# Kernel tuning notes

Measured on AMD Instinct MI355X. Metric: run time of the kernel, lower is better.

The kernel has to match this reference:

```python
import jax, jax.numpy as jnp
import numpy as np

B, J, D = 2048, 22, 128

def setup_inputs() -> dict:
    key = jax.random.key(0)
    k1, k2, k3 = jax.random.split(key, 3)
    src = jax.random.normal(k1, (B, J, D), dtype=jnp.float32)
    W = jax.random.normal(k2, (D, D), dtype=jnp.float32) * (1.0 / np.sqrt(D))
    b = jax.random.normal(k3, (D,), dtype=jnp.float32) * 0.01
    return {"src": src, "W": W, "b": b}

def reference(src, W, b):
    # Path-based accumulation sum_k (src[path[k+1]] - src[path[k]]) telescopes
    # to src[:, j, :] - src[:, i, :] for the shortest path i -> j.
    # pairwise[b, i, j, :] = src[b, j, :] - src[b, i, :]
    pairwise = src[:, None, :, :] - src[:, :, None, :]  # [B, J, J, D]
    # nn.Linear on last dim: x @ W^T + b
    return jnp.einsum('bijd,ed->bije', pairwise, W) + b
```

## Files before the change

kernel.cpp:

```cpp
#include <hip/hip_runtime.h>

#define NB 2048
#define NJ 22
#define ND 128
#define NBAT 8
#define NBLK (NB / NBAT)
#define JD (NJ * ND)
#define ROW4 (JD / 4)

typedef float f32x4 __attribute__((ext_vector_type(4)));

__device__ __forceinline__ void bar_lgkm() {
  asm volatile("s_waitcnt lgkmcnt(0)" ::: "memory");
  __builtin_amdgcn_s_barrier();
  __builtin_amdgcn_sched_barrier(0);
}

__global__ __launch_bounds__(256, 1) void see_kernel(
    const float* __restrict__ src, const float* __restrict__ W,
    const float* __restrict__ bias, float* __restrict__ out) {
  __shared__ float srcS[2][JD];
  __shared__ float YS[JD];

  const int t  = threadIdx.x;
  const int e  = t & 127;
  const int dh = t >> 7;
  const int e4 = t & 31;
  const int j0 = t >> 5;

  float w[64];
  {
    const f32x4* Wrow = reinterpret_cast<const f32x4*>(W + e * ND + dh * 64);
#pragma unroll
    for (int k = 0; k < 16; ++k) {
      f32x4 v = Wrow[k];
      w[4 * k + 0] = v.x; w[4 * k + 1] = v.y;
      w[4 * k + 2] = v.z; w[4 * k + 3] = v.w;
    }
  }
  const f32x4 bb4 = reinterpret_cast<const f32x4*>(bias)[e4];

  const size_t b0 = (size_t)blockIdx.x * NBAT;

  {
    const f32x4* g = reinterpret_cast<const f32x4*>(src + b0 * JD);
    f32x4* l = reinterpret_cast<f32x4*>(&srcS[0][0]);
    f32x4 r0 = g[t], r1 = g[t + 256], r2 = {0, 0, 0, 0};
    if (t < 192) r2 = g[t + 512];
    l[t] = r0; l[t + 256] = r1;
    if (t < 192) l[t + 512] = r2;
  }
  bar_lgkm();

  for (int bi = 0; bi < NBAT; ++bi) {
    const float* sC = &srcS[bi & 1][0];

    float acc[NJ];
#pragma unroll
    for (int j = 0; j < NJ; ++j) {
      const f32x4* s4 = reinterpret_cast<const f32x4*>(sC + j * ND + dh * 64);
      float a = 0.f;
#pragma unroll
      for (int k = 0; k < 16; ++k) {
        f32x4 s = s4[k];
        a += s.x * w[4 * k + 0];
        a += s.y * w[4 * k + 1];
        a += s.z * w[4 * k + 2];
        a += s.w * w[4 * k + 3];
      }
      acc[j] = a;
    }
    if (dh == 0) {
#pragma unroll
      for (int j = 0; j < NJ; ++j) YS[j * ND + e] = acc[j];
    }
    bar_lgkm();
    if (dh == 1) {
#pragma unroll
      for (int j = 0; j < NJ; ++j) YS[j * ND + e] += acc[j];
    }
    bar_lgkm();

    f32x4 p0 = {0,0,0,0}, p1 = {0,0,0,0}, p2 = {0,0,0,0};
    const bool havePf = (bi + 1 < NBAT);
    if (havePf) {
      const f32x4* g = reinterpret_cast<const f32x4*>(src + (b0 + bi + 1) * JD);
      p0 = g[t]; p1 = g[t + 256];
      if (t < 192) p2 = g[t + 512];
    }
    __builtin_amdgcn_sched_barrier(0);

    const f32x4* YS4 = reinterpret_cast<const f32x4*>(YS);
    f32x4 yj0 = YS4[j0 * 32 + e4] + bb4;
    f32x4 yj1 = YS4[(j0 + 8) * 32 + e4] + bb4;
    f32x4 yj2 = {0, 0, 0, 0};
    if (j0 < 6) yj2 = YS4[(j0 + 16) * 32 + e4] + bb4;

    f32x4* outB4 =
        reinterpret_cast<f32x4*>(out + (b0 + bi) * (size_t)NJ * JD);
    for (int ii = 0; ii < NJ; ++ii) {
      f32x4 yi = YS4[ii * 32 + e4];
      f32x4* outRow4 = outB4 + (size_t)ii * ROW4;
      __builtin_nontemporal_store(yj0 - yi, outRow4 + t);
      __builtin_nontemporal_store(yj1 - yi, outRow4 + t + 256);
      if (j0 < 6) __builtin_nontemporal_store(yj2 - yi, outRow4 + t + 512);
    }
    __builtin_amdgcn_sched_barrier(0);

    if (havePf) {
      f32x4* l = reinterpret_cast<f32x4*>(&srcS[(bi + 1) & 1][0]);
      l[t] = p0; l[t + 256] = p1;
      if (t < 192) l[t + 512] = p2;
      bar_lgkm();
    }
  }
}

extern "C" void kernel_launch(void* const* d_in, const int* in_sizes, int n_in,
                              void* d_out, int out_size, void* d_ws, size_t ws_size,
                              hipStream_t stream) {
  const float* src  = (const float*)d_in[0];
  const float* W    = (const float*)d_in[1];
  const float* bias = (const float*)d_in[2];
  float* out = (float*)d_out;

  see_kernel<<<NBLK, 256, 0, stream>>>(src, W, bias, out);
}
```

Before: 113.0 us.

## Preload all batch rows to LDS and split GEMV by rows instead of K

After: 117.4 us. +3.9%, slower.

```diff
diff --git a/kernel.cpp b/kernel.cpp
--- a/kernel.cpp
+++ b/kernel.cpp
@@ -19,76 +19,60 @@
 __global__ __launch_bounds__(256, 1) void see_kernel(
     const float* __restrict__ src, const float* __restrict__ W,
     const float* __restrict__ bias, float* __restrict__ out) {
-  __shared__ float srcS[2][JD];
+  __shared__ float srcS[NBAT][JD];
   __shared__ float YS[JD];
 
-  const int t  = threadIdx.x;
+  const int t = threadIdx.x;
+  const size_t b0 = (size_t)blockIdx.x * NBAT;
+
+#pragma unroll
+  for (int bb = 0; bb < NBAT; ++bb) {
+    const f32x4* g = reinterpret_cast<const f32x4*>(src + (b0 + bb) * JD);
+    f32x4* l = reinterpret_cast<f32x4*>(&srcS[bb][0]);
+    f32x4 r0 = g[t], r1 = g[t + 256], r2 = {0, 0, 0, 0};
+    if (t < 192) r2 = g[t + 512];
+    l[t] = r0; l[t + 256] = r1;
+    if (t < 192) l[t + 512] = r2;
+  }
+
   const int e  = t & 127;
-  const int dh = t >> 7;
-  const int e4 = t & 31;
-  const int j0 = t >> 5;
-
-  float w[64];
+  const int jb = (t >> 7) * 11;
+  float w[128];
   {
-    const f32x4* Wrow = reinterpret_cast<const f32x4*>(W + e * ND + dh * 64);
+    const f32x4* Wrow = reinterpret_cast<const f32x4*>(W + e * ND);
 #pragma unroll
-    for (int k = 0; k < 16; ++k) {
+    for (int k = 0; k < 32; ++k) {
       f32x4 v = Wrow[k];
       w[4 * k + 0] = v.x; w[4 * k + 1] = v.y;
       w[4 * k + 2] = v.z; w[4 * k + 3] = v.w;
     }
   }
+  const int e4 = t & 31;
+  const int j0 = t >> 5;
   const f32x4 bb4 = reinterpret_cast<const f32x4*>(bias)[e4];
 
-  const size_t b0 = (size_t)blockIdx.x * NBAT;
+  for (int bi = 0; bi < NBAT; ++bi) {
+    bar_lgkm();
 
-  {
-    const f32x4* g = reinterpret_cast<const f32x4*>(src + b0 * JD);
-    f32x4* l = reinterpret_cast<f32x4*>(&srcS[0][0]);
-    f32x4 r0 = g[t], r1 = g[t + 256], r2 = {0, 0, 0, 0};
-    if (t < 192) r2 = g[t + 512];
-    l[t] = r0; l[t + 256] = r1;
-    if (t < 192) l[t + 512] = r2;
-  }
-  bar_lgkm();
-
-  for (int bi = 0; bi < NBAT; ++bi) {
-    const float* sC = &srcS[bi & 1][0];
-
-    float acc[NJ];
+    float acc[11];
 #pragma unroll
-    for (int j = 0; j < NJ; ++j) {
-      const f32x4* s4 = reinterpret_cast<const f32x4*>(sC + j * ND + dh * 64);
+    for (int jj = 0; jj < 11; ++jj) {
+      const f32x4* s4 = reinterpret_cast<const f32x4*>(&srcS[bi][(jb + jj) * ND]);
       float a = 0.f;
 #pragma unroll
-      for (int k = 0; k < 16; ++k) {
+      for (int k = 0; k < 32; ++k) {
         f32x4 s = s4[k];
         a += s.x * w[4 * k + 0];
         a += s.y * w[4 * k + 1];
         a += s.z * w[4 * k + 2];
         a += s.w * w[4 * k + 3];
       }
-      acc[j] = a;
+      acc[jj] = a;
     }
-    if (dh == 0) {
 #pragma unroll
-      for (int j = 0; j < NJ; ++j) YS[j * ND + e] = acc[j];
-    }
+    for (int jj = 0; jj < 11; ++jj) YS[(jb + jj) * ND + e] = acc[jj];
+
     bar_lgkm();
-    if (dh == 1) {
-#pragma unroll
-      for (int j = 0; j < NJ; ++j) YS[j * ND + e] += acc[j];
-    }
-    bar_lgkm();
-
-    f32x4 p0 = {0,0,0,0}, p1 = {0,0,0,0}, p2 = {0,0,0,0};
-    const bool havePf = (bi + 1 < NBAT);
-    if (havePf) {
-      const f32x4* g = reinterpret_cast<const f32x4*>(src + (b0 + bi + 1) * JD);
-      p0 = g[t]; p1 = g[t + 256];
-      if (t < 192) p2 = g[t + 512];
-    }
-    __builtin_amdgcn_sched_barrier(0);
 
     const f32x4* YS4 = reinterpret_cast<const f32x4*>(YS);
     f32x4 yj0 = YS4[j0 * 32 + e4] + bb4;
@@ -96,22 +80,13 @@
     f32x4 yj2 = {0, 0, 0, 0};
     if (j0 < 6) yj2 = YS4[(j0 + 16) * 32 + e4] + bb4;
 
-    f32x4* outB4 =
-        reinterpret_cast<f32x4*>(out + (b0 + bi) * (size_t)NJ * JD);
+    f32x4* outB4 = reinterpret_cast<f32x4*>(out + (b0 + bi) * (size_t)NJ * JD);
     for (int ii = 0; ii < NJ; ++ii) {
       f32x4 yi = YS4[ii * 32 + e4];
       f32x4* outRow4 = outB4 + (size_t)ii * ROW4;
-      __builtin_nontemporal_store(yj0 - yi, outRow4 + t);
-      __builtin_nontemporal_store(yj1 - yi, outRow4 + t + 256);
-      if (j0 < 6) __builtin_nontemporal_store(yj2 - yi, outRow4 + t + 512);
-    }
-    __builtin_amdgcn_sched_barrier(0);
-
-    if (havePf) {
-      f32x4* l = reinterpret_cast<f32x4*>(&srcS[(bi + 1) & 1][0]);
-      l[t] = p0; l[t + 256] = p1;
-      if (t < 192) l[t + 512] = p2;
-      bar_lgkm();
+      outRow4[t] = yj0 - yi;
+      outRow4[t + 256] = yj1 - yi;
+      if (j0 < 6) outRow4[t + 512] = yj2 - yi;
     }
   }
 }
```
